# Kernel optimization log

Hardware: AMD Instinct MI355X
Metric: run time of the kernel (lower is better)

## Reference

```python
import jax, jax.numpy as jnp
import numpy as np

B, S, HID = 4, 2048, 1024
NH, L, A = 8, 64, 64           # num_heads, linear_dim, attention_dim
NB = 128                        # time buckets
THETA = 10000.0


def _ln(x, g, b, eps=1e-5):
    m = x.mean(-1, keepdims=True)
    v = ((x - m) ** 2).mean(-1, keepdims=True)
    return (x - m) / jnp.sqrt(v + eps) * g + b


def _ln_na(x, eps=1e-5):  # F.layer_norm without affine
    m = x.mean(-1, keepdims=True)
    v = ((x - m) ** 2).mean(-1, keepdims=True)
    return (x - m) / jnp.sqrt(v + eps)


def _rope(x):
    # x: [B,H,S,A], full-dim interleaved RoPE (rope_partial_dim=0)
    inv = 1.0 / (THETA ** (jnp.arange(0, A, 2, dtype=jnp.float32) / A))
    f = jnp.arange(S, dtype=jnp.float32)[:, None] * inv[None, :]  # [S, A/2]
    cos, sin = jnp.cos(f), jnp.sin(f)
    e, o = x[..., ::2], x[..., 1::2]
    oe = e * cos - o * sin
    oo = o * cos + e * sin
    return jnp.stack([oe, oo], axis=-1).reshape(x.shape)


def setup_inputs() -> dict:
    key = jax.random.key(0)
    ks = jax.random.split(key, 12)
    x = jax.random.normal(ks[0], (B, S, HID), jnp.float32)
    interval = jnp.sort(jax.random.randint(ks[1], (B, S), 0, 1000000), axis=1).astype(jnp.int32)
    attn_mask = jnp.broadcast_to(jnp.tril(jnp.ones((S, S), bool)), (B, S, S))
    next_action_type = jax.random.randint(ks[2], (B, S), 0, 3).astype(jnp.int32)
    next_mask = jax.random.randint(ks[3], (B, S), 0, 2).astype(jnp.int32)
    uvqk = 0.02 * jax.random.normal(ks[4], (HID, 2 * L * NH + 2 * A * NH), jnp.float32)
    o_w = 0.02 * jax.random.normal(ks[5], (L * NH, HID), jnp.float32)
    pos_w = 0.02 * jax.random.normal(ks[6], (2 * S - 1,), jnp.float32)
    ts_w = 0.02 * jax.random.normal(ks[7], (NB + 1,), jnp.float32)
    act_tab = (0.02 * jax.random.normal(ks[8], (4, 32), jnp.float32)).at[0].set(0.0)
    film_w = 0.02 * jax.random.normal(ks[9], (32, 2 * HID), jnp.float32)
    return {
        'x': x, 'interval': interval, 'attn_mask': attn_mask,
        'next_action_type': next_action_type, 'next_mask': next_mask,
        'ln_g': jnp.ones(HID), 'ln_b': jnp.zeros(HID),
        'uvqk': uvqk, 'o_w': o_w, 'o_b': jnp.zeros(HID),
        'pos_w': pos_w, 'ts_w': ts_w, 'act_tab': act_tab,
        'film_ln_g': jnp.ones(32), 'film_ln_b': jnp.zeros(32),
        'film_w': film_w, 'film_b': jnp.zeros(2 * HID),
        'pr_ln_g': jnp.ones(HID), 'pr_ln_b': jnp.zeros(HID),
        'r_scale': jnp.float32(0.1), 'b_scale': jnp.float32(0.1),
    }


def reference(x, interval, attn_mask, next_action_type, next_mask,
              ln_g, ln_b, uvqk, o_w, o_b, pos_w, ts_w, act_tab,
              film_ln_g, film_ln_b, film_w, film_b, pr_ln_g, pr_ln_b,
              r_scale, b_scale):
    h = _ln(x, ln_g, ln_b)
    proj = jax.nn.silu(jnp.einsum('bsh,hd->bsd', h, uvqk))
    U = proj[..., :L * NH]
    V = proj[..., L * NH:2 * L * NH]
    Q = proj[..., 2 * L * NH:2 * L * NH + A * NH]
    K = proj[..., 2 * L * NH + A * NH:]
    U = U.reshape(B, S, NH, L).transpose(0, 2, 1, 3)
    V = V.reshape(B, S, NH, L).transpose(0, 2, 1, 3)
    Q = _rope(Q.reshape(B, S, NH, A).transpose(0, 2, 1, 3))
    K = _rope(K.reshape(B, S, NH, A).transpose(0, 2, 1, 3))
    scores = jnp.einsum('bhsa,bhta->bhst', Q, K)  # [B,H,S,S]
    # bucketized time-interval bias (indices are constants, .detach in torch)
    ts = interval.astype(jnp.float32)
    ext = jnp.concatenate([ts, ts[:, S - 1:S]], axis=1)  # [B, S+1]
    diff = ext[:, 1:, None] - ext[:, None, :-1]          # [B, S, S]
    bucket = jnp.clip((jnp.log(jnp.clip(jnp.abs(diff), 1.0, None)) / 0.301).astype(jnp.int32), 0, NB)
    scores = scores + ts_w[bucket][:, None]
    # relative position bias: bias[i,j] = pos_w[S-1 + j - i]
    rel_idx = jnp.arange(S)[None, :] - jnp.arange(S)[:, None] + (S - 1)
    scores = scores + pos_w[rel_idx][None, None]
    scores = jax.nn.silu(scores) / S
    scores = jnp.where(attn_mask[:, None], scores, 0.0)
    out = _ln_na(jnp.einsum('bhst,bhtl->bhsl', scores, V))
    u_dot = (U * out).transpose(0, 2, 1, 3).reshape(B, S, NH * L)
    outputs = x + u_dot @ o_w + o_b
    # PinRec FiLM gating
    ids = (next_action_type + 1) * (next_mask == 1)
    ae = act_tab[ids]                                    # [B,S,32]
    rb = _ln(ae, film_ln_g, film_ln_b) @ film_w + film_b
    r, b = rb[..., :HID], rb[..., HID:]
    outputs = outputs + _ln(outputs, pr_ln_g, pr_ln_b) * jnp.tanh(r) * r_scale + b * b_scale
    return outputs
```

## Files before the change

kernel.cpp:

```cpp
#include <hip/hip_runtime.h>
#include <hip/hip_bf16.h>
#include <stdint.h>

#define B_    4
#define S_    2048
#define HID_  1024
#define NH_   8
#define L_    64
#define A_    64
#define NB_   128

using bf16 = __hip_bfloat16;
typedef __bf16 bf16x8 __attribute__((ext_vector_type(8)));
typedef float  f32x4  __attribute__((ext_vector_type(4)));

__device__ __forceinline__ float bf2f(bf16 v){ return __bfloat162float(v); }
__device__ __forceinline__ bf16  f2bf(float v){ return __float2bfloat16(v); }

__device__ __forceinline__ f32x4 mfma16(bf16x8 a, bf16x8 b, f32x4 c){
  return __builtin_amdgcn_mfma_f32_16x16x32_bf16(a, b, c, 0, 0, 0);
}

__device__ __forceinline__ void gll16(const void* g, void* l){
  __builtin_amdgcn_global_load_lds(
      (const __attribute__((address_space(1))) unsigned int*)g,
      (__attribute__((address_space(3))) unsigned int*)l, 16, 0, 0);
}

__global__ __launch_bounds__(256) void k_tcast(const float* __restrict__ src,
                                               bf16* __restrict__ dst, int R, int C){
  __shared__ float t[32][33];
  int c0 = blockIdx.x*32, r0 = blockIdx.y*32;
  int tx = threadIdx.x & 31, ty = threadIdx.x >> 5;
#pragma unroll
  for (int j=0;j<4;j++) t[ty+j*8][tx] = src[(size_t)(r0+ty+j*8)*C + c0+tx];
  __syncthreads();
#pragma unroll
  for (int j=0;j<4;j++) dst[(size_t)(c0+ty+j*8)*R + r0+tx] = f2bf(t[tx][ty+j*8]);
}

__global__ void k_rb4(const float* __restrict__ act_tab, const float* __restrict__ fg,
                      const float* __restrict__ fb, const float* __restrict__ fw,
                      const float* __restrict__ fbias, float* __restrict__ rb4){
  __shared__ float lnae[4][32];
  __shared__ float mv[4][2];
  int tid = threadIdx.x;
  if (tid < 128) lnae[tid>>5][tid&31] = act_tab[tid];
  __syncthreads();
  if (tid < 4){
    float s=0.f, q=0.f;
#pragma unroll
    for (int i=0;i<32;i++){ float a=lnae[tid][i]; s+=a; q+=a*a; }
    float mean = s*(1.f/32.f);
    mv[tid][0] = mean;
    mv[tid][1] = rsqrtf(q*(1.f/32.f) - mean*mean + 1e-5f);
  }
  __syncthreads();
  if (tid < 128){
    int id=tid>>5, i=tid&31;
    lnae[id][i] = (lnae[id][i]-mv[id][0])*mv[id][1]*fg[i] + fb[i];
  }
  __syncthreads();
  for (int idx=tid; idx<4*2048; idx+=256){
    int id = idx>>11, j = idx&2047;
    float acc = fbias[j];
#pragma unroll
    for (int i=0;i<32;i++) acc += lnae[id][i]*fw[i*2048+j];
    rb4[idx] = acc;
  }
}

__global__ __launch_bounds__(256) void k_ln_x(const float* __restrict__ x,
      const float* __restrict__ g, const float* __restrict__ bta, bf16* __restrict__ h){
  int row = blockIdx.x; int tid = threadIdx.x;
  const float* xr = x + (size_t)row*HID_;
  float v[4]; float sum=0.f, sq=0.f;
#pragma unroll
  for (int i=0;i<4;i++){ v[i]=xr[tid + i*256]; sum+=v[i]; sq+=v[i]*v[i]; }
#pragma unroll
  for (int o=1;o<64;o<<=1){ sum+=__shfl_xor(sum,o,64); sq+=__shfl_xor(sq,o,64); }
  __shared__ float red[2][4];
  int wid=tid>>6, lane=tid&63;
  if(lane==0){ red[0][wid]=sum; red[1][wid]=sq; }
  __syncthreads();
  sum = red[0][0]+red[0][1]+red[0][2]+red[0][3];
  sq  = red[1][0]+red[1][1]+red[1][2]+red[1][3];
  float mean = sum*(1.f/HID_);
  float rstd = rsqrtf(sq*(1.f/HID_)-mean*mean + 1e-5f);
#pragma unroll
  for (int i=0;i<4;i++){
    int c = tid+i*256;
    h[(size_t)row*HID_ + c] = f2bf((v[i]-mean)*rstd*g[c] + bta[c]);
  }
}

__global__ __launch_bounds__(256) void k_gemm_uvqk(const bf16* __restrict__ hb,
        const bf16* __restrict__ wT, bf16* __restrict__ proj){
  __shared__ __align__(16) ushort shA[128*32];
  __shared__ __align__(16) ushort shB[128*32];
  const int K = 1024;
  int bx = blockIdx.x;
  int tm = bx & 63, tn = bx >> 6;
  int brow = tm*128, bcol = tn*128;
  int tid = threadIdx.x;
  int wid = tid>>6, lane = tid&63, lr = lane&15, lg = lane>>4;
  int wm = wid>>1, wn = wid&1;
  f32x4 acc[4][4] = {};
  for (int k0=0; k0<K; k0+=32){
    __syncthreads();
#pragma unroll
    for (int i=0;i<2;i++){
      int c = tid + i*256;
      int row = c>>2, kp = (c&3)*8;
      gll16(&hb[(size_t)(brow+row)*K + k0+kp], &shA[c*8]);
      gll16(&wT[(size_t)(bcol+row)*K + k0+kp], &shB[c*8]);
    }
    __syncthreads();
    bf16x8 a[4], b[4];
#pragma unroll
    for (int m=0;m<4;m++) a[m] = *(const bf16x8*)&shA[(wm*64+m*16+lr)*32 + lg*8];
#pragma unroll
    for (int n=0;n<4;n++) b[n] = *(const bf16x8*)&shB[(wn*64+n*16+lr)*32 + lg*8];
#pragma unroll
    for (int m=0;m<4;m++)
#pragma unroll
      for (int n=0;n<4;n++)
        acc[m][n] = mfma16(a[m], b[n], acc[m][n]);
  }
#pragma unroll
  for (int m=0;m<4;m++)
#pragma unroll
    for (int n=0;n<4;n++)
#pragma unroll
      for (int r=0;r<4;r++){
        int row = brow + wm*64+m*16+lg*4+r;
        int col = bcol + wn*64+n*16+lr;
        float v = acc[m][n][r];
        proj[(size_t)row*2048 + col] = f2bf(v / (1.f + __expf(-v)));
      }
}

__global__ __launch_bounds__(256) void k_rope(bf16* __restrict__ proj){
  int row = blockIdx.x;
  int s = row & (S_-1);
  int t = threadIdx.x;
  int h = t >> 5, p = t & 31;
  const float L2_10000 = 13.287712379549449f;
  float inv = exp2f(-(float)p * (L2_10000/32.f));
  float f = (float)s * inv;
  float sn, c; sincosf(f, &sn, &c);
  size_t base = (size_t)row*2048;
  int cq = 1024 + h*64 + 2*p;
  float qe = bf2f(proj[base+cq]), qo = bf2f(proj[base+cq+1]);
  proj[base+cq]   = f2bf(qe*c - qo*sn);
  proj[base+cq+1] = f2bf(qo*c + qe*sn);
  int ck = 1536 + h*64 + 2*p;
  float ke = bf2f(proj[base+ck]), ko = bf2f(proj[base+ck+1]);
  proj[base+ck]   = f2bf(ke*c - ko*sn);
  proj[base+ck+1] = f2bf(ko*c + ke*sn);
}

__global__ __launch_bounds__(256) void k_vtrans(const bf16* __restrict__ proj, bf16* __restrict__ Vt){
  __shared__ __align__(16) ushort lds[32][520];
  int bx = blockIdx.x; int b = bx>>6; int s0 = (bx&63)*32;
  int tid = threadIdx.x;
#pragma unroll
  for (int i=0;i<8;i++){
    int c = tid + i*256;
    int sl = c>>6, e8 = (c&63)*8;
    *(uint4*)&lds[sl][e8] = *(const uint4*)&proj[((size_t)(b*S_+s0+sl))*2048 + 512 + e8];
  }
  __syncthreads();
#pragma unroll
  for (int q=0;q<2;q++){
    int hl = tid + q*256;
    ushort v[32];
#pragma unroll
    for (int j=0;j<32;j++) v[j] = lds[j][hl];
#pragma unroll
    for (int w=0;w<4;w++)
      *(uint4*)&Vt[((size_t)b*512 + hl)*S_ + s0 + w*8] = *(uint4*)&v[w*8];
  }
}

__global__ __launch_bounds__(256) void k_bias_sw(const int* __restrict__ interval,
      const float* __restrict__ ts_w, const float* __restrict__ pos_w,
      bf16* __restrict__ bsw){
  __shared__ int   itvL[2048];
  __shared__ float posL[2080];
  __shared__ float tsL[132];
  int bx = blockIdx.x;
  int b  = bx & 3;
  int st = 63 - (bx >> 2);
  int tid = threadIdx.x, wid = tid>>6, lane = tid&63, lr = lane&15, lg = lane>>4;
  const int* itv = interval + b*S_;
  for (int i=tid;i<2048;i+=256) itvL[i]=itv[i];
  int pbase = 2016 - st*32;
  int plen  = st*32 + 63;
  for (int i=tid;i<plen;i+=256) posL[i] = pos_w[pbase + i];
  if (tid<129) tsL[tid]=ts_w[tid];
  __syncthreads();
  size_t tbase = (size_t)b*2080 + (size_t)(st*(st+1)/2);
  for (int tt = wid; tt <= st; tt += 4){
    ushort ov[16];
#pragma unroll
    for (int m=0;m<2;m++)
#pragma unroll
      for (int n=0;n<2;n++)
#pragma unroll
        for (int r=0;r<4;r++){
          int sl = m*16 + lg*4 + r;
          int sg = st*32 + sl;
          int tg = tt*32 + n*16 + lr;
          float val;
          if (tg <= sg){
            int sp = sg+1; if (sp>2047) sp=2047;
            float d = fmaxf(fabsf((float)(itvL[sp]-itvL[tg])),1.f);
            int bk = (int)(__log2f(d)*2.3027481f);
            bk = bk<0?0:(bk>NB_?NB_:bk);
            val = tsL[bk] + posL[tg - sl + 31];
          } else val = -10000.f;
          ov[m*8+n*4+r] = __bfloat16_as_ushort(f2bf(val));
        }
    bf16* dst = bsw + ((tbase + tt)*64 + lane)*16;
    *(uint4*)dst     = *(uint4*)&ov[0];
    *(uint4*)(dst+8) = *(uint4*)&ov[8];
  }
}

__global__ __launch_bounds__(256, 6) void k_attn(const bf16* __restrict__ proj,
     const bf16* __restrict__ Vt, const bf16* __restrict__ bsw,
     bf16* __restrict__ u_dot){
  __shared__ __align__(16) bf16 Plds[4][32][36];
  __shared__ float redbuf[4][16][65];
  int bx = blockIdx.x;
  int st = 63 - (bx >> 5);
  int b  = (bx >> 3) & 3;
  int h  = bx & 7;
  int s0 = st*32;
  int tid = threadIdx.x, wid = tid>>6, lane = tid&63, lr = lane&15, lg = lane>>4;
  size_t rowb = (size_t)b * S_;

  bf16x8 aq[2][2];
#pragma unroll
  for (int m=0;m<2;m++)
#pragma unroll
    for (int ks=0;ks<2;ks++)
      aq[m][ks] = *(const bf16x8*)&proj[(rowb + s0 + m*16 + lr)*2048 + 1024 + h*64 + ks*32 + lg*8];

  size_t tbase = (size_t)b*2080 + (size_t)(st*(st+1)/2);
  f32x4 acc[2][4] = {};
  int nT = st + 1;
  for (int tt = wid; tt < nT; tt += 4){
    int t0 = tt*32;
    bf16x8 kb[2][2];
#pragma unroll
    for (int n=0;n<2;n++)
#pragma unroll
      for (int ks=0;ks<2;ks++)
        kb[n][ks] = *(const bf16x8*)&proj[(rowb + t0 + n*16 + lr)*2048 + 1536 + h*64 + ks*32 + lg*8];
    const bf16* bp = bsw + ((tbase + tt)*64 + lane)*16;
    bf16x8 bb0 = *(const bf16x8*)bp;
    bf16x8 bb1 = *(const bf16x8*)(bp+8);
    f32x4 sacc[2][2] = {};
#pragma unroll
    for (int m=0;m<2;m++)
#pragma unroll
      for (int n=0;n<2;n++)
#pragma unroll
        for (int ks=0;ks<2;ks++)
          sacc[m][n] = mfma16(aq[m][ks], kb[n][ks], sacc[m][n]);
#pragma unroll
    for (int m=0;m<2;m++)
#pragma unroll
      for (int n=0;n<2;n++)
#pragma unroll
        for (int r=0;r<4;r++){
          float bv = bf2f(m ? (bf16)bb1[n*4+r] : (bf16)bb0[n*4+r]);
          float v  = sacc[m][n][r] + bv;
          float p  = v * __builtin_amdgcn_rcpf(1.f + __expf(-v));
          Plds[wid][m*16 + lg*4 + r][n*16 + lr] = f2bf(p);
        }
    bf16x8 pa[2];
#pragma unroll
    for (int m=0;m<2;m++) pa[m] = *(const bf16x8*)&Plds[wid][m*16+lr][lg*8];
#pragma unroll
    for (int n=0;n<4;n++){
      bf16x8 bv = *(const bf16x8*)&Vt[((size_t)b*512 + h*64 + n*16+lr)*S_ + t0 + lg*8];
#pragma unroll
      for (int m=0;m<2;m++)
        acc[m][n] = mfma16(pa[m], bv, acc[m][n]);
    }
  }

#pragma unroll
  for (int m=0;m<2;m++){
    __syncthreads();
#pragma unroll
    for (int n=0;n<4;n++)
#pragma unroll
      for (int r=0;r<4;r++)
        redbuf[wid][lg*4+r][n*16+lr] = acc[m][n][r];
    __syncthreads();
#pragma unroll
    for (int q=0;q<4;q++){
      int rr = wid*4 + q;
      float v = (redbuf[0][rr][lane] + redbuf[1][rr][lane]
               + redbuf[2][rr][lane] + redbuf[3][rr][lane]) * (1.f/(float)S_);
      float sum = v, sq = v*v;
#pragma unroll
      for (int o=1;o<64;o<<=1){ sum += __shfl_xor(sum,o,64); sq += __shfl_xor(sq,o,64); }
      float mean = sum*(1.f/64.f);
      float rstd = rsqrtf(sq*(1.f/64.f) - mean*mean + 1e-5f);
      int sg = s0 + m*16 + rr;
      float u = bf2f(proj[(rowb+sg)*2048 + h*64 + lane]);
      u_dot[(rowb+sg)*512 + h*64 + lane] = f2bf((v-mean)*rstd*u);
    }
  }
}

__global__ __launch_bounds__(256) void k_gemm_out(const bf16* __restrict__ ud,
        const bf16* __restrict__ wT, const float* __restrict__ x,
        const float* __restrict__ ob, float* __restrict__ out){
  __shared__ __align__(16) ushort shA[128*32];
  __shared__ __align__(16) ushort shB[128*32];
  const int K = 512;
  int bx = blockIdx.x;
  int tm = bx & 63, tn = bx >> 6;
  int brow = tm*128, bcol = tn*128;
  int tid = threadIdx.x;
  int wid = tid>>6, lane = tid&63, lr = lane&15, lg = lane>>4;
  int wm = wid>>1, wn = wid&1;
  f32x4 acc[4][4] = {};
  for (int k0=0; k0<K; k0+=32){
    __syncthreads();
#pragma unroll
    for (int i=0;i<2;i++){
      int c = tid + i*256;
      int row = c>>2, kp = (c&3)*8;
      gll16(&ud[(size_t)(brow+row)*K + k0+kp], &shA[c*8]);
      gll16(&wT[(size_t)(bcol+row)*K + k0+kp], &shB[c*8]);
    }
    __syncthreads();
    bf16x8 a[4], b[4];
#pragma unroll
    for (int m=0;m<4;m++) a[m] = *(const bf16x8*)&shA[(wm*64+m*16+lr)*32 + lg*8];
#pragma unroll
    for (int n=0;n<4;n++) b[n] = *(const bf16x8*)&shB[(wn*64+n*16+lr)*32 + lg*8];
#pragma unroll
    for (int m=0;m<4;m++)
#pragma unroll
      for (int n=0;n<4;n++)
        acc[m][n] = mfma16(a[m], b[n], acc[m][n]);
  }
#pragma unroll
  for (int m=0;m<4;m++)
#pragma unroll
    for (int n=0;n<4;n++)
#pragma unroll
      for (int r=0;r<4;r++){
        int row = brow + wm*64+m*16+lg*4+r;
        int col = bcol + wn*64+n*16+lr;
        out[(size_t)row*HID_ + col] = acc[m][n][r] + x[(size_t)row*HID_ + col] + ob[col];
      }
}

__global__ __launch_bounds__(256) void k_film(float* __restrict__ out,
   const float* __restrict__ rb4, const int* __restrict__ nat, const int* __restrict__ nm,
   const float* __restrict__ prg, const float* __restrict__ prb,
   const float* __restrict__ rsp, const float* __restrict__ bsp){
  int row = blockIdx.x; int tid = threadIdx.x;
  float* orow = out + (size_t)row*HID_;
  int id = (nat[row] + 1) * (nm[row]==1 ? 1 : 0);
  float rs = rsp[0], bs = bsp[0];
  float v[4]; float sum=0.f, sq=0.f;
#pragma unroll
  for (int i=0;i<4;i++){ v[i]=orow[tid+i*256]; sum+=v[i]; sq+=v[i]*v[i]; }
#pragma unroll
  for (int o=1;o<64;o<<=1){ sum+=__shfl_xor(sum,o,64); sq+=__shfl_xor(sq,o,64); }
  __shared__ float red[2][4];
  int wid=tid>>6, lane=tid&63;
  if(lane==0){ red[0][wid]=sum; red[1][wid]=sq; }
  __syncthreads();
  sum = red[0][0]+red[0][1]+red[0][2]+red[0][3];
  sq  = red[1][0]+red[1][1]+red[1][2]+red[1][3];
  float mean = sum*(1.f/HID_);
  float rstd = rsqrtf(sq*(1.f/HID_)-mean*mean + 1e-5f);
#pragma unroll
  for (int i=0;i<4;i++){
    int c = tid+i*256;
    float ln = (v[i]-mean)*rstd*prg[c]+prb[c];
    float r  = rb4[id*2048 + c];
    float b2 = rb4[id*2048 + 1024 + c];
    orow[c] = v[i] + ln*tanhf(r)*rs + b2*bs;
  }
}

extern "C" void kernel_launch(void* const* d_in, const int* in_sizes, int n_in,
                              void* d_out, int out_size, void* d_ws, size_t ws_size,
                              hipStream_t stream){
  const float* x        = (const float*)d_in[0];
  const int*   interval = (const int*)d_in[1];
  const int*   nat      = (const int*)d_in[3];
  const int*   nm       = (const int*)d_in[4];
  const float* ln_g     = (const float*)d_in[5];
  const float* ln_b     = (const float*)d_in[6];
  const float* uvqk     = (const float*)d_in[7];
  const float* o_w      = (const float*)d_in[8];
  const float* o_b      = (const float*)d_in[9];
  const float* pos_w    = (const float*)d_in[10];
  const float* ts_w     = (const float*)d_in[11];
  const float* act_tab  = (const float*)d_in[12];
  const float* film_g   = (const float*)d_in[13];
  const float* film_bt  = (const float*)d_in[14];
  const float* film_w   = (const float*)d_in[15];
  const float* film_b   = (const float*)d_in[16];
  const float* pr_g     = (const float*)d_in[17];
  const float* pr_b     = (const float*)d_in[18];
  const float* r_scale  = (const float*)d_in[19];
  const float* b_scale  = (const float*)d_in[20];
  float* out = (float*)d_out;

  char* ws = (char*)d_ws;
  bf16*  uvqkT = (bf16*)(ws);
  bf16*  o_wT  = (bf16*)(ws + (4u<<20));
  float* rb4   = (float*)(ws + (5u<<20));
  bf16*  hb    = (bf16*)(ws + (6u<<20));
  bf16*  Vt    = (bf16*)(ws + (6u<<20));
  bf16*  ud    = (bf16*)(ws + (14u<<20));
  bf16*  proj  = (bf16*)(ws + (22u<<20));
  bf16*  bsw   = (bf16*)(ws + (54u<<20));

  k_tcast<<<dim3(2048/32, 1024/32), 256, 0, stream>>>(uvqk, uvqkT, 1024, 2048);
  k_tcast<<<dim3(1024/32,  512/32), 256, 0, stream>>>(o_w,  o_wT,   512, 1024);
  k_rb4<<<1, 256, 0, stream>>>(act_tab, film_g, film_bt, film_w, film_b, rb4);
  k_bias_sw<<<256, 256, 0, stream>>>(interval, ts_w, pos_w, bsw);
  k_ln_x<<<B_*S_, 256, 0, stream>>>(x, ln_g, ln_b, hb);
  k_gemm_uvqk<<<64*16, 256, 0, stream>>>(hb, uvqkT, proj);
  k_rope<<<B_*S_, 256, 0, stream>>>(proj);
  k_vtrans<<<B_*64, 256, 0, stream>>>(proj, Vt);
  k_attn<<<64*32, 256, 0, stream>>>(proj, Vt, bsw, ud);
  k_gemm_out<<<64*8, 256, 0, stream>>>(ud, o_wT, x, o_b, out);
  k_film<<<B_*S_, 256, 0, stream>>>(out, rb4, nat, nm, pr_g, pr_b, r_scale, b_scale);
}
```

Before: 254.8 us.

## Alias attention LDS buffers, raise occupancy, reorder grid and prefetch V

The attention kernel now keeps the P tile and the reduction buffer in one shared allocation, which reduces LDS per block, and raises the launch-bounds occupancy hint from 6 to 8 blocks. The block index mapping is reordered so that the head is the slowest-varying index and batch and query tile vary within it. V tile loads are hoisted ahead of the QK MFMAs so their latency overlaps the score computation. The cost is more register pressure from holding the V fragments and the tighter register budget at 8 blocks, which could cause spills. The LDS aliasing depends on the first __syncthreads in the reduction loop to keep the two uses apart.

New measurement: 458.6 us. 1.8x slower.

```diff
diff --git a/kernel.cpp b/kernel.cpp
--- a/kernel.cpp
+++ b/kernel.cpp
@@ -228,15 +228,17 @@
   }
 }
 
-__global__ __launch_bounds__(256, 6) void k_attn(const bf16* __restrict__ proj,
+__global__ __launch_bounds__(256, 8) void k_attn(const bf16* __restrict__ proj,
      const bf16* __restrict__ Vt, const bf16* __restrict__ bsw,
      bf16* __restrict__ u_dot){
-  __shared__ __align__(16) bf16 Plds[4][32][36];
-  __shared__ float redbuf[4][16][65];
+  __shared__ __align__(16) char smem[16640];
+  bf16  (*Plds)[32][36]  = (bf16 (*)[32][36])smem;
+  float (*redbuf)[16][65] = (float(*)[16][65])smem;
   int bx = blockIdx.x;
-  int st = 63 - (bx >> 5);
-  int b  = (bx >> 3) & 3;
-  int h  = bx & 7;
+  int h  = bx >> 8;
+  int r  = bx & 255;
+  int b  = r & 3;
+  int st = 63 - (r >> 2);
   int s0 = st*32;
   int tid = threadIdx.x, wid = tid>>6, lane = tid&63, lr = lane&15, lg = lane>>4;
   size_t rowb = (size_t)b * S_;
@@ -262,6 +264,10 @@
     const bf16* bp = bsw + ((tbase + tt)*64 + lane)*16;
     bf16x8 bb0 = *(const bf16x8*)bp;
     bf16x8 bb1 = *(const bf16x8*)(bp+8);
+    bf16x8 bv[4];
+#pragma unroll
+    for (int n=0;n<4;n++)
+      bv[n] = *(const bf16x8*)&Vt[((size_t)b*512 + h*64 + n*16+lr)*S_ + t0 + lg*8];
     f32x4 sacc[2][2] = {};
 #pragma unroll
     for (int m=0;m<2;m++)
@@ -275,22 +281,20 @@
 #pragma unroll
       for (int n=0;n<2;n++)
 #pragma unroll
-        for (int r=0;r<4;r++){
-          float bv = bf2f(m ? (bf16)bb1[n*4+r] : (bf16)bb0[n*4+r]);
-          float v  = sacc[m][n][r] + bv;
+        for (int r2=0;r2<4;r2++){
+          float bvv = bf2f(m ? (bf16)bb1[n*4+r2] : (bf16)bb0[n*4+r2]);
+          float v  = sacc[m][n][r2] + bvv;
           float p  = v * __builtin_amdgcn_rcpf(1.f + __expf(-v));
-          Plds[wid][m*16 + lg*4 + r][n*16 + lr] = f2bf(p);
+          Plds[wid][m*16 + lg*4 + r2][n*16 + lr] = f2bf(p);
         }
     bf16x8 pa[2];
 #pragma unroll
     for (int m=0;m<2;m++) pa[m] = *(const bf16x8*)&Plds[wid][m*16+lr][lg*8];
 #pragma unroll
-    for (int n=0;n<4;n++){
-      bf16x8 bv = *(const bf16x8*)&Vt[((size_t)b*512 + h*64 + n*16+lr)*S_ + t0 + lg*8];
+    for (int n=0;n<4;n++)
 #pragma unroll
       for (int m=0;m<2;m++)
-        acc[m][n] = mfma16(pa[m], bv, acc[m][n]);
-    }
+        acc[m][n] = mfma16(pa[m], bv[n], acc[m][n]);
   }
 
 #pragma unroll
@@ -299,8 +303,8 @@
 #pragma unroll
     for (int n=0;n<4;n++)
 #pragma unroll
-      for (int r=0;r<4;r++)
-        redbuf[wid][lg*4+r][n*16+lr] = acc[m][n][r];
+      for (int r2=0;r2<4;r2++)
+        redbuf[wid][lg*4+r2][n*16+lr] = acc[m][n][r2];
     __syncthreads();
 #pragma unroll
     for (int q=0;q<4;q++){
```
